# Kernel optimization log

Hardware: AMD Instinct MI355X
Metric: run time of the kernel (lower is better)

The kernel has to match this reference:

```python
import jax, jax.numpy as jnp
import numpy as np
from jax import lax

NK = 21   # num_kernels / predicted kernel size
MK = 21   # max_kernel_size
B, H, W = 8, 256, 256


def _make_gauss_weight():
    """Fixed bank: identity kernel + 21 FFT-inverse gaussian kernels, repeated x3 channels."""
    def gauss1d(ws, sigma):
        xs = np.arange(ws)
        g = np.exp(-(xs - ws // 2) ** 2 / (2.0 * sigma ** 2))
        return g / g.sum()

    def inv_kernel(ws, sigma):
        g = gauss1d(ws, sigma)
        w2 = np.outer(g, g)
        K = np.fft.fft2(w2)
        K = np.conj(K) / (np.abs(K) ** 2 + 0.01)
        return np.abs(np.fft.ifft2(K))

    w = np.zeros((NK + 1, 1, MK, MK), np.float32)
    ks = 3
    for i in range(NK):
        pad = (MK - ks) // 2
        w[i + 1, 0, pad:pad + ks, pad:pad + ks] = inv_kernel(ks, 0.25 * (i + 1))
        if i >= 2 and i % 2 == 0 and ks < MK:
            ks += 2
    w[0, 0, MK // 2, MK // 2] = 1.0  # identity (delta) kernel
    return np.repeat(w, 3, axis=0)   # (66, 1, 21, 21)


def conv(x, w, pad, groups=1, b=None):
    y = lax.conv_general_dilated(
        x, w, (1, 1), [(pad, pad), (pad, pad)],
        dimension_numbers=("NCHW", "OIHW", "NCHW"),
        feature_group_count=groups)
    if b is not None:
        y = y + b[None, :, None, None]
    return y


def adaptive_avg_pool(x, oh, ow):
    """Matches torch AdaptiveAvgPool2d bin boundaries (static shapes)."""
    Hh, Ww = x.shape[2], x.shape[3]
    def bins(L, o):
        return [((i * L) // o, -((-(i + 1) * L) // o)) for i in range(o)]
    rows = []
    for (hs, he) in bins(Hh, oh):
        cols = [x[:, :, hs:he, ws:we].mean(axis=(2, 3)) for (ws, we) in bins(Ww, ow)]
        rows.append(jnp.stack(cols, axis=-1))
    return jnp.stack(rows, axis=-2)  # (N, C, oh, ow)


def setup_inputs() -> dict:
    key = jax.random.key(0)
    ks = jax.random.split(key, 12)
    s = 0.02
    return {
        "x": jax.random.normal(ks[0], (B, 3, H, W), jnp.float32),
        "w_gauss": jnp.asarray(_make_gauss_weight()),
        "p1_w": jax.random.normal(ks[1], (128, 3, 11, 11), jnp.float32) * s,
        "p1_b": jax.random.normal(ks[2], (128,), jnp.float32) * s,
        "p2_w": jax.random.normal(ks[3], (441, 128, 1, 1), jnp.float32) * s,
        "p3_w": jax.random.normal(ks[4], (441, 441, 1, 1), jnp.float32) * s,
        "cs_w": jax.random.normal(ks[5], (3, 3, 3, 3), jnp.float32) * s,
        "cs_b": jax.random.normal(ks[6], (3,), jnp.float32) * s,
        "tr_w": jax.random.normal(ks[7], (66, 3, 3, 3), jnp.float32) * s,
        "tr_b": jax.random.normal(ks[8], (66,), jnp.float32) * s,
        "fu_w": jax.random.normal(ks[9], (66, 132, 3, 3), jnp.float32) * s,
        "fu_b": jax.random.normal(ks[10], (66,), jnp.float32) * s,
    }


def reference(x, w_gauss, p1_w, p1_b, p2_w, p3_w, cs_w, cs_b, tr_w, tr_b, fu_w, fu_b):
    b = x.shape[0]
    pad = (NK - 1) // 2  # 10

    # fixed inverse-gaussian blur bank, grouped over the 3 input channels -> (B,66,H,W)
    x_gauss = conv(x, w_gauss, pad, groups=3)

    # Predictor: per-sample 3x21x21 dynamic kernel
    h = jax.nn.leaky_relu(conv(x, p1_w, 2, b=p1_b), 0.2)
    h = adaptive_avg_pool(h, 3, 3)
    h = jax.nn.leaky_relu(conv(h, p2_w, 0), 0.2)
    h = adaptive_avg_pool(h, 3, 1)           # (B,441,3,1)
    h = jax.nn.softmax(conv(h, p3_w, 0), axis=1)
    kern = h.reshape(b, 3, NK, NK)           # per-sample predicted kernel

    # batched per-sample dynamic conv: groups=B trick replaces the python loop
    xr = x.reshape(1, b * 3, x.shape[2], x.shape[3])
    out = conv(xr, kern, pad, groups=b)      # (1,B,H,W)
    output = jnp.broadcast_to(out.reshape(b, 1, x.shape[2], x.shape[3]), x.shape)

    ax_out = conv(x, cs_w, 1, b=cs_b)                       # (B,3,H,W)
    x_af = conv(output, tr_w, 1, b=tr_b)                    # (B,66,H,W)
    fused = conv(jnp.concatenate([x_gauss, x_af], axis=1), fu_w, 1, b=fu_b)  # (B,66,H,W)
    return (fused, ax_out)
```

## Files before the change

### kernel.cpp

```cpp
#include <hip/hip_runtime.h>
#include <hip/hip_bf16.h>

#define BB 8
#define HH 256
#define WW 256
#define HW 65536

typedef __attribute__((ext_vector_type(8))) short bf16x8;
typedef __attribute__((ext_vector_type(4))) float f32x4;
typedef __attribute__((ext_vector_type(8))) unsigned short u16x8;
#define MFMA16(a, b, c) __builtin_amdgcn_mfma_f32_16x16x32_bf16(a, b, c, 0, 0, 0)

__device__ __forceinline__ ushort f2bf(float f) {
  union { float f; uint32_t u; } c; c.f = f;
  uint32_t r = (c.u + 0x7fffu + ((c.u >> 16) & 1u)) >> 16;
  return (ushort)r;
}

#define OFF_XG    0
#define OFF_PP    25165824
#define OFF_BP    34603008
#define OFF_XGN   69206016
#define OFF_OUT1  144703488
#define OFF_KERN  146837504
#define OFF_BW    146880000
#define OFF_BWZ   147018240
#define OFF_BIAS  147126784
#define OFF_TB    147127296
#define OFF_T     147129856

__global__ __launch_bounds__(256) void k_prepA(const float* __restrict__ fuw,
                                               const float* __restrict__ trw,
                                               const float* __restrict__ trb,
                                               const float* __restrict__ p1w,
                                               float* __restrict__ T,
                                               float* __restrict__ TB,
                                               ushort* __restrict__ Bw,
                                               ushort* __restrict__ Bp) {
  int i = blockIdx.x * 256 + threadIdx.x;
  if (i < 5346) {
    int o = i / 81, a = (i / 9) % 9, s = i % 9;
    float acc = 0.f;
    for (int cp = 0; cp < 66; ++cp)
      acc += fuw[(o * 132 + 66 + cp) * 9 + a] *
             (trw[(cp * 3) * 9 + s] + trw[(cp * 3 + 1) * 9 + s] + trw[(cp * 3 + 2) * 9 + s]);
    T[i] = acc; return;
  }
  i -= 5346;
  if (i < 594) {
    int o = i / 9, a = i % 9;
    float acc = 0.f;
    for (int cp = 0; cp < 66; ++cp) acc += trb[cp] * fuw[(o * 132 + 66 + cp) * 9 + a];
    TB[i] = acc; return;
  }
  i -= 594;
  if (i < 2 * 9 * 80 * 32) {
    int cc = i / 23040, t = (i / 2560) % 9, o = (i / 32) % 80, kl = i & 31;
    int c = cc * 32 + kl;
    Bw[i] = (o < 66) ? f2bf(fuw[(o * 132 + c) * 9 + t]) : 0;
    return;
  }
  i -= 2 * 9 * 80 * 32;
  if (i < 16 * 128 * 32) {
    int kc = i / 4096, o = (i / 32) % 128, kl = i & 31;
    int k = kc * 32 + kl;
    float v = 0.f;
    if (k < 484) { int u = k / 44, r2 = k % 44, vv = r2 / 4, c = r2 & 3;
                   if (c < 3) v = p1w[(o * 3 + c) * 121 + u * 11 + vv]; }
    Bp[i] = f2bf(v);
    return;
  }
}

__device__ __forceinline__ float W5val(int o, int d, const float* T) {
  int dy = d / 5, dx = d % 5;
  float acc = 0.f;
  for (int ua = 0; ua < 3; ++ua) {
    int us = dy - ua; if (us < 0 || us > 2) continue;
    for (int va = 0; va < 3; ++va) {
      int vs = dx - va; if (vs < 0 || vs > 2) continue;
      acc += T[(o * 9 + ua * 3 + va) * 9 + us * 3 + vs];
    }
  }
  return acc;
}

__global__ __launch_bounds__(256) void k_prepB(const float* __restrict__ fuw,
                                               const float* __restrict__ fub,
                                               const float* __restrict__ T,
                                               const float* __restrict__ TB,
                                               ushort* __restrict__ BwZ,
                                               float* __restrict__ bias_tot) {
  int i = blockIdx.x * 256 + threadIdx.x;
  if (i < 5120) {
    int zc = i / 2560, o = (i / 32) % 80, s = i & 31;
    float v = 0.f;
    if (o < 66) {
      if (zc == 0) {
        if (s < 18) { int ch = 64 + s / 9, a = s % 9; v = fuw[(o * 132 + ch) * 9 + a]; }
        else        { v = W5val(o, s - 18, T); }
      } else {
        if (s < 11) v = W5val(o, 14 + s, T);
      }
    }
    BwZ[i] = f2bf(v); return;
  }
  i -= 5120;
  if (i < 80) {
    float v = 0.f;
    if (i < 66) { v = fub[i]; for (int a = 0; a < 9; ++a) v += TB[i * 9 + a]; }
    bias_tot[i] = v;
  }
}

template <int KS>
__device__ __forceinline__ void xg_conv(const float* __restrict__ xt,
                                        const float* __restrict__ wgp,
                                        float* a, int r, int wq) {
  constexpr int P0 = (21 - KS) / 2;
  constexpr int Q0 = P0 & ~3;
  constexpr int D0 = P0 - Q0;
  constexpr int NL = ((P0 + KS + 6) >> 2) - (P0 >> 2) + 1;
#pragma unroll 1
  for (int kh = P0; kh < P0 + KS; ++kh) {
    float rx[NL * 4];
    const int F0 = (r + kh) * 320 + 8 * wq + Q0;
#pragma unroll
    for (int i = 0; i < NL; ++i) {
      int Fi = F0 + 4 * i;
      *(float4*)(rx + 4 * i) = *(const float4*)(xt + (Fi ^ (((Fi >> 5) & 1) << 2)));
    }
    const float* wr = wgp + kh * 21 + P0;
#pragma unroll
    for (int t = 0; t < KS; ++t) {
      float wv = wr[t];
#pragma unroll
      for (int u = 0; u < 8; ++u) a[u] += wv * rx[D0 + t + u];
    }
  }
}

__global__ __launch_bounds__(256, 4) void k_xgauss(const float* __restrict__ x,
                                                   const float* __restrict__ wg,
                                                   __hip_bfloat16* __restrict__ xg) {
  const int bu = blockIdx.z;
  const int b = bu / 24, u = bu % 24;
  const int g = u >> 3;
  const int j = (u & 7) + 7 * g;
  const int h0 = blockIdx.y * 8;
  __shared__ __align__(16) float xt[28 * 320];
  const float* xp = x + (b * 3 + g) * HW;
  for (int e = threadIdx.x; e < 28 * 320; e += 256) {
    int row = e / 320, col = e % 320;
    int gy = h0 + row - 10, gx = col - 10;
    float v = (gy >= 0 && gy < HH && gx >= 0 && gx < WW) ? xp[gy * WW + gx] : 0.f;
    xt[e ^ (((e >> 5) & 1) << 2)] = v;
  }
  __syncthreads();
  int i_ = j - 1;
  int im = (i_ - 1 > 0) ? (i_ - 1) : 0;
  const int ks = (j == 0) ? 1 : 3 + 2 * (im >> 1);
  const int wq = threadIdx.x & 31, r = threadIdx.x >> 5;
  const float* wgp = wg + (3 * j) * 441;
  float a[8] = {0.f, 0.f, 0.f, 0.f, 0.f, 0.f, 0.f, 0.f};
  switch (ks) {
    case 1:  xg_conv<1>(xt, wgp, a, r, wq); break;
    case 3:  xg_conv<3>(xt, wgp, a, r, wq); break;
    case 5:  xg_conv<5>(xt, wgp, a, r, wq); break;
    case 7:  xg_conv<7>(xt, wgp, a, r, wq); break;
    case 9:  xg_conv<9>(xt, wgp, a, r, wq); break;
    case 11: xg_conv<11>(xt, wgp, a, r, wq); break;
    case 13: xg_conv<13>(xt, wgp, a, r, wq); break;
    case 15: xg_conv<15>(xt, wgp, a, r, wq); break;
    case 17: xg_conv<17>(xt, wgp, a, r, wq); break;
    case 19: xg_conv<19>(xt, wgp, a, r, wq); break;
    default: xg_conv<21>(xt, wgp, a, r, wq); break;
  }
  u16x8 ov;
#pragma unroll
  for (int k = 0; k < 8; ++k) ov[k] = f2bf(a[k]);
  int oidx = (bu * HW) + (h0 + r) * WW + 8 * wq;
  *(u16x8*)((ushort*)xg + oidx) = ov;
}

__global__ __launch_bounds__(256) void k_tr(const ushort* __restrict__ xg,
                                            ushort* __restrict__ xgn) {
  __shared__ ushort ls[64 * 72];
  int p0 = blockIdx.x * 64;
  int b = p0 >> 16, sp = p0 & 65535;
  for (int e = threadIdx.x; e < 72 * 64; e += 256) {
    int c = e >> 6, i = e & 63;
    int uc = c / 3 + c / 22;
    ls[i * 72 + c] = (c < 66) ? xg[(size_t)(b * 24 + uc) * HW + sp + i] : (ushort)0;
  }
  __syncthreads();
  for (int e = threadIdx.x; e < 576; e += 256) {
    *(float4*)(xgn + (size_t)p0 * 72 + e * 8) = *(const float4*)(ls + e * 8);
  }
}

__global__ __launch_bounds__(1024, 4) void k_pmm(const float* __restrict__ x,
                                                 const ushort* __restrict__ Bp,
                                                 const float* __restrict__ p1b,
                                                 float* __restrict__ pp) {
  __shared__ __align__(16) float xt2[3840];
  __shared__ float ps[4 * 1152];
  const int b = blockIdx.z, h0 = blockIdx.y * 16, w0 = blockIdx.x * 16;
  const int tid = threadIdx.x, wave = tid >> 6, lane = tid & 63;
  const int m = lane & 15, q = lane >> 4;
  for (int e = tid; e < 4608; e += 1024) ps[e] = 0.f;
  if (tid < 676) {
    int py = tid / 26, pxc = tid % 26, gy = h0 - 2 + py, gx = w0 - 2 + pxc;
    float4 v = make_float4(0.f, 0.f, 0.f, 0.f);
    if (gy >= 0 && gy < HH && gx >= 0 && gx < WW) {
      const float* xb = x + b * 3 * HW + gy * WW + gx;
      v.x = xb[0]; v.y = xb[HW]; v.z = xb[2 * HW];
    }
    *(float4*)(xt2 + tid * 4) = v;
  }
  for (int e = tid; e < 1136; e += 1024) xt2[2704 + e] = 0.f;
  f32x4 acc[8];
#pragma unroll
  for (int n = 0; n < 8; ++n) acc[n] = (f32x4){0.f, 0.f, 0.f, 0.f};
  __syncthreads();
  const int q8 = q * 8;
  const float* afb = xt2 + (wave * 26 + m) * 4;
#pragma unroll
  for (int kc = 0; kc < 16; ++kc) {
    const int s = kc * 32 + q8;
    const int u = (s * 745) >> 15;
    const int rem = s - 44 * u;
    const int a0 = s + 60 * u;
    const int a1 = a0 + ((rem == 40) ? 64 : 4);
    float4 lo = *(const float4*)(afb + a0);
    float4 hi = *(const float4*)(afb + a1);
    union { ushort us[8]; bf16x8 v; } af;
    af.us[0] = f2bf(lo.x); af.us[1] = f2bf(lo.y);
    af.us[2] = f2bf(lo.z); af.us[3] = f2bf(lo.w);
    af.us[4] = f2bf(hi.x); af.us[5] = f2bf(hi.y);
    af.us[6] = f2bf(hi.z); af.us[7] = f2bf(hi.w);
    bf16x8 bf[8];
#pragma unroll
    for (int nt = 0; nt < 8; ++nt)
      bf[nt] = *(const bf16x8*)(Bp + ((kc * 128 + nt * 16 + m) * 32 + q8));
#pragma unroll
    for (int nt = 0; nt < 8; ++nt)
      acc[nt] = MFMA16(af.v, bf[nt], acc[nt]);
  }
  float bv[8];
#pragma unroll
  for (int nt = 0; nt < 8; ++nt) bv[nt] = p1b[nt * 16 + m];
  const int h = h0 + wave;
  float* psq = ps + q * 1152;
  if (h < 250) {
    bool h0m = h < 84, h1m = (h >= 83 && h < 167), h2m = h >= 166;
#pragma unroll
    for (int r = 0; r < 4; ++r) {
      int w = w0 + (q << 2) + r;
      if (w >= 250) continue;
      bool w0m = w < 84, w1m = (w >= 83 && w < 167), w2m = w >= 166;
#pragma unroll
      for (int nt = 0; nt < 8; ++nt) {
        int o = (nt << 4) + m;
        float vz = acc[nt][r] + bv[nt];
        vz = vz >= 0.f ? vz : 0.2f * vz;
        if (h0m) { if (w0m) atomicAdd(&psq[o], vz);        if (w1m) atomicAdd(&psq[128 + o], vz);
                   if (w2m) atomicAdd(&psq[256 + o], vz); }
        if (h1m) { if (w0m) atomicAdd(&psq[384 + o], vz);  if (w1m) atomicAdd(&psq[512 + o], vz);
                   if (w2m) atomicAdd(&psq[640 + o], vz); }
        if (h2m) { if (w0m) atomicAdd(&psq[768 + o], vz);  if (w1m) atomicAdd(&psq[896 + o], vz);
                   if (w2m) atomicAdd(&psq[1024 + o], vz); }
      }
    }
  }
  __syncthreads();
  const int tile = blockIdx.y * 16 + blockIdx.x;
  float* dst = pp + (size_t)(b * 256 + tile) * 1152;
  for (int e = tid; e < 1152; e += 1024) {
    int idx = (e % 9) * 128 + (e / 9);
    dst[e] = ps[idx] + ps[1152 + idx] + ps[2304 + idx] + ps[3456 + idx];
  }
}

__global__ __launch_bounds__(256) void k_pred2(const float* __restrict__ pp,
                                               const float* __restrict__ p2w,
                                               const float* __restrict__ p3w,
                                               float* __restrict__ kernw) {
  const int b = blockIdx.x;
  const int tid = threadIdx.x;
  __shared__ float hin[1152];
  __shared__ float h2p[1323];
  __shared__ float h3l[1323];
  __shared__ float mx[3], sm[3];
  for (int e = tid; e < 1152; e += 256) {
    float s = 0.f;
    const float* qp = pp + (size_t)b * 256 * 1152 + e;
#pragma unroll 4
    for (int t = 0; t < 256; ++t) s += qp[t * 1152];
    hin[e] = s * (1.f / 7056.f);
  }
  __syncthreads();
  for (int c = tid; c < 441; c += 256) {
    float z[9] = {0.f,0.f,0.f,0.f,0.f,0.f,0.f,0.f,0.f};
    const float* wr = p2w + c * 128;
    for (int k = 0; k < 128; k++) {
      float wv = wr[k];
      const float* hp = &hin[k * 9];
#pragma unroll
      for (int p = 0; p < 9; p++) z[p] += wv * hp[p];
    }
#pragma unroll
    for (int i = 0; i < 3; i++) {
      float s = 0.f;
#pragma unroll
      for (int jj = 0; jj < 3; jj++) {
        float zz = z[i * 3 + jj];
        s += (zz >= 0.f) ? zz : 0.2f * zz;
      }
      h2p[c * 3 + i] = s * (1.f / 3.f);
    }
  }
  __syncthreads();
  for (int c = tid; c < 441; c += 256) {
    float a0 = 0.f, a1 = 0.f, a2 = 0.f;
    const float* wr = p3w + c * 441;
    for (int k = 0; k < 441; k++) {
      float wv = wr[k];
      a0 += wv * h2p[k * 3];
      a1 += wv * h2p[k * 3 + 1];
      a2 += wv * h2p[k * 3 + 2];
    }
    h3l[c * 3] = a0; h3l[c * 3 + 1] = a1; h3l[c * 3 + 2] = a2;
  }
  __syncthreads();
  if (tid < 3) {
    float mxv = -1e30f;
    for (int c = 0; c < 441; c++) mxv = fmaxf(mxv, h3l[c * 3 + tid]);
    float s = 0.f;
    for (int c = 0; c < 441; c++) s += expf(h3l[c * 3 + tid] - mxv);
    mx[tid] = mxv; sm[tid] = 1.f / s;
  }
  __syncthreads();
  for (int f = tid; f < 1323; f += 256) {
    int i = f % 3;
    kernw[b * 1323 + f] = expf(h3l[f] - mx[i]) * sm[i];
  }
}

__global__ __launch_bounds__(256) void k_dyn(const float* __restrict__ x,
                                             const float* __restrict__ kernw,
                                             float* __restrict__ out1) {
  const int b = blockIdx.z;
  const int h0 = blockIdx.y * 16, w0 = blockIdx.x * 64;
  __shared__ float kl[1323];
  __shared__ float xt[3 * 36 * 84];
  for (int e = threadIdx.x; e < 1323; e += 256) kl[e] = kernw[b * 1323 + e];
  for (int e = threadIdx.x; e < 3 * 36 * 84; e += 256) {
    int ci = e / 3024, rem = e % 3024;
    int ty = rem / 84, tx = rem % 84;
    int gy = h0 + ty - 10, gx = w0 + tx - 10;
    xt[e] = (gy >= 0 && gy < HH && gx >= 0 && gx < WW)
                ? x[(b * 3 + ci) * HW + gy * WW + gx] : 0.f;
  }
  __syncthreads();
  const int wq = threadIdx.x & 15, r = threadIdx.x >> 4;
  float a0 = 0.f, a1 = 0.f, a2 = 0.f, a3 = 0.f;
  for (int ci = 0; ci < 3; ci++) {
    for (int kh = 0; kh < 21; kh++) {
      float rx[24];
      const float4* rp = (const float4*)&xt[ci * 3024 + (r + kh) * 84 + 4 * wq];
      float4* rv = (float4*)rx;
#pragma unroll
      for (int i = 0; i < 6; i++) rv[i] = rp[i];
      const float* wr = &kl[ci * 441 + kh * 21];
#pragma unroll
      for (int kw = 0; kw < 21; kw++) {
        float wv = wr[kw];
        a0 += wv * rx[kw];     a1 += wv * rx[kw + 1];
        a2 += wv * rx[kw + 2]; a3 += wv * rx[kw + 3];
      }
    }
  }
  int idx = b * HW + (h0 + r) * WW + w0 + 4 * wq;
  *(float4*)&out1[idx] = make_float4(a0, a1, a2, a3);
}

__global__ __launch_bounds__(256) void k_ax(const float* __restrict__ x,
                                            const float* __restrict__ csw,
                                            const float* __restrict__ csb,
                                            float* __restrict__ out2) {
  int idx = blockIdx.x * 256 + threadIdx.x;
  if (idx >= BB * 3 * HW) return;
  int w = idx & 255, h = (idx >> 8) & 255;
  int oc = (idx >> 16) % 3, b = idx / (3 * HW);
  float acc = csb[oc];
  for (int ic = 0; ic < 3; ic++) {
    const float* xc = x + (b * 3 + ic) * HW;
    const float* wp = csw + (oc * 3 + ic) * 9;
#pragma unroll
    for (int u = 0; u < 3; u++) {
      int iy = h + u - 1;
      if (iy < 0 || iy >= HH) continue;
#pragma unroll
      for (int v = 0; v < 3; v++) {
        int ix = w + v - 1;
        if (ix >= 0 && ix < WW) acc += xc[iy * WW + ix] * wp[u * 3 + v];
      }
    }
  }
  out2[idx] = acc;
}

__global__ __launch_bounds__(256, 3) void k_fmma(const ushort* __restrict__ xgn,
                                                 const float* __restrict__ out1,
                                                 const ushort* __restrict__ Bw,
                                                 const ushort* __restrict__ BwZ,
                                                 const float* __restrict__ bias_tot,
                                                 float* __restrict__ outf) {
  __shared__ __align__(16) char smem[40080];
  ushort* xs  = (ushort*)smem;
  float*  o1s = (float*)(smem + 20736);
  ushort* xs2 = (ushort*)(smem + 22336);
  ushort* az  = (ushort*)(smem + 23632);
  float*  st  = (float*)(smem + 23632);
  const int b = blockIdx.z, h0 = blockIdx.y * 16, w0 = blockIdx.x * 16;
  const int tid = threadIdx.x, wave = tid >> 6, lane = tid & 63;
  const int m = lane & 15, q = lane >> 4;
  f32x4 acc[4][5];
#pragma unroll
  for (int a = 0; a < 4; ++a)
#pragma unroll
    for (int n = 0; n < 5; ++n) acc[a][n] = (f32x4){0.f, 0.f, 0.f, 0.f};

  for (int cc = 0; cc < 2; ++cc) {
    __syncthreads();
    for (int e = tid; e < 1296; e += 256) {
      int u = e & 3, p = e >> 2, py = p / 18, px = p % 18;
      int gy = h0 - 1 + py, gx = w0 - 1 + px;
      float4 v = make_float4(0.f, 0.f, 0.f, 0.f);
      if (gy >= 0 && gy < HH && gx >= 0 && gx < WW)
        v = *(const float4*)(xgn + (size_t)(b * HW + gy * WW + gx) * 72 + cc * 32 + u * 8);
      *(float4*)(xs + p * 32 + u * 8) = v;
    }
    __syncthreads();
#pragma unroll
    for (int t = 0; t < 9; ++t) {
      const int u = t / 3, v = t % 3;
      bf16x8 bf[5];
#pragma unroll
      for (int nt = 0; nt < 5; ++nt)
        bf[nt] = *(const bf16x8*)(Bw + (((cc * 9 + t) * 80 + nt * 16 + m) * 32 + q * 8));
#pragma unroll
      for (int mt = 0; mt < 4; ++mt) {
        int row = (wave << 2) + mt;
        bf16x8 af = *(const bf16x8*)(xs + ((row + u) * 18 + m + v) * 32 + q * 8);
#pragma unroll
        for (int nt = 0; nt < 5; ++nt)
          acc[mt][nt] = MFMA16(af, bf[nt], acc[mt][nt]);
      }
    }
  }
  __syncthreads();
  for (int e = tid; e < 324; e += 256) {
    int py = e / 18, px = e % 18, gy = h0 - 1 + py, gx = w0 - 1 + px;
    uint32_t v = 0;
    if (gy >= 0 && gy < HH && gx >= 0 && gx < WW)
      v = *(const uint32_t*)(xgn + (size_t)(b * HW + gy * WW + gx) * 72 + 64);
    *(uint32_t*)(xs2 + e * 2) = v;
  }
  for (int e = tid; e < 400; e += 256) {
    int py = e / 20, px = e % 20, gy = h0 - 2 + py, gx = w0 - 2 + px;
    o1s[e] = (gy >= 0 && gy < HH && gx >= 0 && gx < WW) ? out1[b * HW + gy * WW + gx] : 0.f;
  }
  __syncthreads();
  const int bpy = tid >> 4, bpx = tid & 15;
#pragma unroll
  for (int zc = 0; zc < 2; ++zc) {
    union { ushort us[32]; float4 f4[4]; } vals;
    if (zc == 0) {
#pragma unroll
      for (int s = 0; s < 18; ++s) {
        int ch = s / 9, a = s % 9, u = a / 3, v = a % 3;
        vals.us[s] = xs2[((bpy + u) * 18 + bpx + v) * 2 + ch];
      }
#pragma unroll
      for (int d = 0; d < 14; ++d)
        vals.us[18 + d] = f2bf(o1s[(bpy + d / 5) * 20 + bpx + d % 5]);
    } else {
#pragma unroll
      for (int s = 0; s < 11; ++s) {
        int d = 14 + s;
        vals.us[s] = f2bf(o1s[(bpy + d / 5) * 20 + bpx + d % 5]);
      }
#pragma unroll
      for (int s = 11; s < 32; ++s) vals.us[s] = 0;
    }
    __syncthreads();
#pragma unroll
    for (int u = 0; u < 4; ++u)
      *(float4*)(az + tid * 32 + ((u ^ (tid & 3)) << 3)) = vals.f4[u];
    __syncthreads();
    bf16x8 bf[5];
#pragma unroll
    for (int nt = 0; nt < 5; ++nt)
      bf[nt] = *(const bf16x8*)(BwZ + ((zc * 80 + nt * 16 + m) * 32 + q * 8));
#pragma unroll
    for (int mt = 0; mt < 4; ++mt) {
      int px = (((wave << 2) + mt) << 4) + m;
      bf16x8 af = *(const bf16x8*)(az + px * 32 + ((q ^ (px & 3)) << 3));
#pragma unroll
      for (int nt = 0; nt < 5; ++nt)
        acc[mt][nt] = MFMA16(af, bf[nt], acc[mt][nt]);
    }
  }
#pragma unroll 1
  for (int nt = 0; nt < 5; ++nt) {
    __syncthreads();
#pragma unroll
    for (int mt = 0; mt < 4; ++mt) {
      int pxb = (((wave << 2) + mt) << 4);
#pragma unroll
      for (int r = 0; r < 4; ++r)
        st[m * 257 + pxb + q * 4 + r] = acc[mt][nt][r];
    }
    __syncthreads();
#pragma unroll
    for (int kk = 0; kk < 16; ++kk) {
      int o = nt * 16 + kk;
      if (o < 66) {
        float bvv = bias_tot[o];
        outf[((b * 66 + o) * HH + h0 + (tid >> 4)) * WW + w0 + (tid & 15)] =
            st[kk * 257 + tid] + bvv;
      }
    }
  }
}

__global__ __launch_bounds__(256) void k_fix(const float* __restrict__ out1,
                                             const float* __restrict__ T,
                                             const float* __restrict__ TB,
                                             float* __restrict__ outf) {
  int idx = blockIdx.x * 256 + threadIdx.x;
  if (idx >= 8 * 1020 * 66) return;
  int b = idx / (1020 * 66);
  int rem = idx % (1020 * 66);
  int pi = rem / 66, o = rem % 66;
  int ph, pw;
  if (pi < 256)      { ph = 0;        pw = pi; }
  else if (pi < 512) { ph = 255;      pw = pi - 256; }
  else if (pi < 766) { ph = pi - 511; pw = 0; }
  else               { ph = pi - 765; pw = 255; }
  float corr = 0.f;
#pragma unroll
  for (int a = 0; a < 9; ++a) {
    int ua = a / 3, va = a % 3;
    int qh = ph + ua - 1, qw = pw + va - 1;
    if (qh >= 0 && qh < HH && qw >= 0 && qw < WW) continue;
    float s = TB[o * 9 + a];
#pragma unroll
    for (int t2 = 0; t2 < 9; ++t2) {
      int rh = qh + t2 / 3 - 1, rw = qw + t2 % 3 - 1;
      if (rh >= 0 && rh < HH && rw >= 0 && rw < WW)
        s += out1[b * HW + rh * WW + rw] * T[(o * 9 + a) * 9 + t2];
    }
    corr += s;
  }
  outf[((b * 66 + o) * HH + ph) * WW + pw] -= corr;
}

extern "C" void kernel_launch(void* const* d_in, const int* in_sizes, int n_in,
                              void* d_out, int out_size, void* d_ws, size_t ws_size,
                              hipStream_t stream) {
  const float* x   = (const float*)d_in[0];
  const float* wg  = (const float*)d_in[1];
  const float* p1w = (const float*)d_in[2];
  const float* p1b = (const float*)d_in[3];
  const float* p2w = (const float*)d_in[4];
  const float* p3w = (const float*)d_in[5];
  const float* csw = (const float*)d_in[6];
  const float* csb = (const float*)d_in[7];
  const float* trw = (const float*)d_in[8];
  const float* trb = (const float*)d_in[9];
  const float* fuw = (const float*)d_in[10];
  const float* fub = (const float*)d_in[11];
  float* outf = (float*)d_out;
  float* out2 = outf + 34603008;
  char* ws = (char*)d_ws;
  __hip_bfloat16* xg = (__hip_bfloat16*)(ws + OFF_XG);
  float* pp      = (float*)(ws + OFF_PP);
  ushort* Bp     = (ushort*)(ws + OFF_BP);
  ushort* xgn    = (ushort*)(ws + OFF_XGN);
  float* out1    = (float*)(ws + OFF_OUT1);
  float* kernw   = (float*)(ws + OFF_KERN);
  ushort* Bw     = (ushort*)(ws + OFF_BW);
  ushort* BwZ    = (ushort*)(ws + OFF_BWZ);
  float* biasT   = (float*)(ws + OFF_BIAS);
  float* TBp     = (float*)(ws + OFF_TB);
  float* Tp      = (float*)(ws + OFF_T);

  hipLaunchKernelGGL(k_prepA, dim3(460), dim3(256), 0, stream,
                     fuw, trw, trb, p1w, Tp, TBp, Bw, Bp);
  hipLaunchKernelGGL(k_prepB, dim3(21), dim3(256), 0, stream,
                     fuw, fub, Tp, TBp, BwZ, biasT);
  hipLaunchKernelGGL(k_xgauss, dim3(1, 32, 8 * 24), dim3(256), 0, stream, x, wg, xg);
  hipLaunchKernelGGL(k_tr, dim3(8192), dim3(256), 0, stream, (const ushort*)xg, xgn);
  hipLaunchKernelGGL(k_pmm, dim3(16, 16, 8), dim3(1024), 0, stream, x, Bp, p1b, pp);
  hipLaunchKernelGGL(k_pred2, dim3(8), dim3(256), 0, stream, pp, p2w, p3w, kernw);
  hipLaunchKernelGGL(k_dyn, dim3(4, 16, 8), dim3(256), 0, stream, x, kernw, out1);
  hipLaunchKernelGGL(k_fmma, dim3(16, 16, 8), dim3(256), 0, stream,
                     xgn, out1, Bw, BwZ, biasT, outf);
  hipLaunchKernelGGL(k_fix, dim3(2104), dim3(256), 0, stream, out1, Tp, TBp, outf);
  hipLaunchKernelGGL(k_ax, dim3(6144), dim3(256), 0, stream, x, csw, csb, out2);
}
```

Baseline: 1.499 ms.

## Reuse B fragments across four row tiles per wave in predictor conv

The predictor's 11x11 conv kernel now uses 256-thread blocks where each wave computes four output rows. Each B-fragment load from global memory is reused across four MFMA row tiles instead of one. The input tile is converted to bf16 once at staging time rather than on every A-fragment load, which halves shared-memory footprint and removes repeated conversions. In exchange, register pressure rises to 128 accumulator floats per lane, and the block has fewer waves to hide latency.

```diff
diff --git a/kernel.cpp b/kernel.cpp
--- a/kernel.cpp
+++ b/kernel.cpp
@@ -199,60 +199,64 @@
   }
 }
 
-__global__ __launch_bounds__(1024, 4) void k_pmm(const float* __restrict__ x,
-                                                 const ushort* __restrict__ Bp,
-                                                 const float* __restrict__ p1b,
-                                                 float* __restrict__ pp) {
-  __shared__ __align__(16) float xt2[3840];
+__global__ __launch_bounds__(256, 2) void k_pmm(const float* __restrict__ x,
+                                                const ushort* __restrict__ Bp,
+                                                const float* __restrict__ p1b,
+                                                float* __restrict__ pp) {
+  __shared__ __align__(16) ushort xtb[2880];
   __shared__ float ps[4 * 1152];
   const int b = blockIdx.z, h0 = blockIdx.y * 16, w0 = blockIdx.x * 16;
   const int tid = threadIdx.x, wave = tid >> 6, lane = tid & 63;
   const int m = lane & 15, q = lane >> 4;
-  for (int e = tid; e < 4608; e += 1024) ps[e] = 0.f;
-  if (tid < 676) {
-    int py = tid / 26, pxc = tid % 26, gy = h0 - 2 + py, gx = w0 - 2 + pxc;
-    float4 v = make_float4(0.f, 0.f, 0.f, 0.f);
+  for (int e = tid; e < 4608; e += 256) ps[e] = 0.f;
+  for (int e = tid; e < 676; e += 256) {
+    int py = e / 26, pxc = e % 26, gy = h0 - 2 + py, gx = w0 - 2 + pxc;
+    ushort4 v = make_ushort4(0, 0, 0, 0);
     if (gy >= 0 && gy < HH && gx >= 0 && gx < WW) {
       const float* xb = x + b * 3 * HW + gy * WW + gx;
-      v.x = xb[0]; v.y = xb[HW]; v.z = xb[2 * HW];
-    }
-    *(float4*)(xt2 + tid * 4) = v;
-  }
-  for (int e = tid; e < 1136; e += 1024) xt2[2704 + e] = 0.f;
-  f32x4 acc[8];
-#pragma unroll
-  for (int n = 0; n < 8; ++n) acc[n] = (f32x4){0.f, 0.f, 0.f, 0.f};
+      v.x = f2bf(xb[0]); v.y = f2bf(xb[HW]); v.z = f2bf(xb[2 * HW]);
+    }
+    *(ushort4*)(xtb + e * 4) = v;
+  }
+  for (int e = tid; e < 176; e += 256) xtb[2704 + e] = 0;
+  f32x4 acc[4][8];
+#pragma unroll
+  for (int a = 0; a < 4; ++a)
+#pragma unroll
+    for (int n = 0; n < 8; ++n) acc[a][n] = (f32x4){0.f, 0.f, 0.f, 0.f};
   __syncthreads();
   const int q8 = q * 8;
-  const float* afb = xt2 + (wave * 26 + m) * 4;
 #pragma unroll
   for (int kc = 0; kc < 16; ++kc) {
+    bf16x8 bf[8];
+#pragma unroll
+    for (int nt = 0; nt < 8; ++nt)
+      bf[nt] = *(const bf16x8*)(Bp + ((kc * 128 + nt * 16 + m) * 32 + q8));
     const int s = kc * 32 + q8;
     const int u = (s * 745) >> 15;
     const int rem = s - 44 * u;
     const int a0 = s + 60 * u;
     const int a1 = a0 + ((rem == 40) ? 64 : 4);
-    float4 lo = *(const float4*)(afb + a0);
-    float4 hi = *(const float4*)(afb + a1);
-    union { ushort us[8]; bf16x8 v; } af;
-    af.us[0] = f2bf(lo.x); af.us[1] = f2bf(lo.y);
-    af.us[2] = f2bf(lo.z); af.us[3] = f2bf(lo.w);
-    af.us[4] = f2bf(hi.x); af.us[5] = f2bf(hi.y);
-    af.us[6] = f2bf(hi.z); af.us[7] = f2bf(hi.w);
-    bf16x8 bf[8];
-#pragma unroll
-    for (int nt = 0; nt < 8; ++nt)
-      bf[nt] = *(const bf16x8*)(Bp + ((kc * 128 + nt * 16 + m) * 32 + q8));
-#pragma unroll
-    for (int nt = 0; nt < 8; ++nt)
-      acc[nt] = MFMA16(af.v, bf[nt], acc[nt]);
+#pragma unroll
+    for (int mt = 0; mt < 4; ++mt) {
+      const int row = (wave << 2) + mt;
+      const ushort* ab = xtb + (row * 26 + m) * 4;
+      union { ushort us[8]; bf16x8 v; } af;
+      *(ushort4*)(af.us)     = *(const ushort4*)(ab + a0);
+      *(ushort4*)(af.us + 4) = *(const ushort4*)(ab + a1);
+#pragma unroll
+      for (int nt = 0; nt < 8; ++nt)
+        acc[mt][nt] = MFMA16(af.v, bf[nt], acc[mt][nt]);
+    }
   }
   float bv[8];
 #pragma unroll
   for (int nt = 0; nt < 8; ++nt) bv[nt] = p1b[nt * 16 + m];
-  const int h = h0 + wave;
   float* psq = ps + q * 1152;
-  if (h < 250) {
+#pragma unroll
+  for (int mt = 0; mt < 4; ++mt) {
+    int h = h0 + (wave << 2) + mt;
+    if (h >= 250) continue;
     bool h0m = h < 84, h1m = (h >= 83 && h < 167), h2m = h >= 166;
 #pragma unroll
     for (int r = 0; r < 4; ++r) {
@@ -262,7 +266,7 @@
 #pragma unroll
       for (int nt = 0; nt < 8; ++nt) {
         int o = (nt << 4) + m;
-        float vz = acc[nt][r] + bv[nt];
+        float vz = acc[mt][nt][r] + bv[nt];
         vz = vz >= 0.f ? vz : 0.2f * vz;
         if (h0m) { if (w0m) atomicAdd(&psq[o], vz);        if (w1m) atomicAdd(&psq[128 + o], vz);
                    if (w2m) atomicAdd(&psq[256 + o], vz); }
@@ -276,7 +280,7 @@
   __syncthreads();
   const int tile = blockIdx.y * 16 + blockIdx.x;
   float* dst = pp + (size_t)(b * 256 + tile) * 1152;
-  for (int e = tid; e < 1152; e += 1024) {
+  for (int e = tid; e < 1152; e += 256) {
     int idx = (e % 9) * 128 + (e / 9);
     dst[e] = ps[idx] + ps[1152 + idx] + ps[2304 + idx] + ps[3456 + idx];
   }
@@ -604,7 +608,7 @@
                      fuw, fub, Tp, TBp, BwZ, biasT);
   hipLaunchKernelGGL(k_xgauss, dim3(1, 32, 8 * 24), dim3(256), 0, stream, x, wg, xg);
   hipLaunchKernelGGL(k_tr, dim3(8192), dim3(256), 0, stream, (const ushort*)xg, xgn);
-  hipLaunchKernelGGL(k_pmm, dim3(16, 16, 8), dim3(1024), 0, stream, x, Bp, p1b, pp);
+  hipLaunchKernelGGL(k_pmm, dim3(16, 16, 8), dim3(256), 0, stream, x, Bp, p1b, pp);
   hipLaunchKernelGGL(k_pred2, dim3(8), dim3(256), 0, stream, pp, p2w, p3w, kernw);
   hipLaunchKernelGGL(k_dyn, dim3(4, 16, 8), dim3(256), 0, stream, x, kernw, out1);
   hipLaunchKernelGGL(k_fmma, dim3(16, 16, 8), dim3(256), 0, stream,
```

New measurement: 1.345 ms. 1.12x faster.
